# Kernel tuning notes

Measured on AMD Instinct MI355X. Metric: run time of the kernel, lower is better.

Reference implementation:

```python
import jax, jax.numpy as jnp
import numpy as np

B, C, P, N_PARTS, JOINTS_PER_PART = 2048, 256, 15, 5, 3
GROUPS = 4
EPS = 1e-5
MASK_VAL = 10000.0


def setup_inputs() -> dict:
    key = jax.random.key(0)
    k1, k2, k3 = jax.random.split(key, 3)
    g = (2 * C) // GROUPS  # 128
    return {
        "x": jax.random.normal(k1, (B, C, P, 1), jnp.float32),
        "conv_w": jax.random.normal(k2, (GROUPS, g, g), jnp.float32) * 0.05,
        "conv_b": jax.random.normal(k3, (2 * C,), jnp.float32) * 0.05,
        "bn_gamma": jnp.ones((2 * C,), jnp.float32),
        "bn_beta": jnp.zeros((2 * C,), jnp.float32),
    }


def reference(x, conv_w, conv_b, bn_gamma, bn_beta):
    Bb, Cc, Pp, _ = x.shape
    xs = x[..., 0]  # [B, C, P]

    # relative[b,c,i,k] = xs[b,c,k] - xs[b,c,i]; for a row i in part p the
    # reduction is max_k(relative - MASK_VAL * [k in part p]). Since the mask
    # only depends on the part of row i, precompute the per-part masked max of
    # xs over k and broadcast-subtract xs[i].
    part_id = jnp.arange(Pp) // JOINTS_PER_PART  # [P]
    Mg = jnp.where(part_id[None, :] == jnp.arange(N_PARTS)[:, None], -MASK_VAL, 0.0)  # [5, P]
    m = jnp.max(xs[:, :, None, :] + Mg[None, None, :, :], axis=-1)  # [B, C, 5]
    tmp = m[:, :, part_id] - xs  # [B, C, P]

    y = jnp.concatenate([xs, tmp], axis=1)  # [B, 2C, P]

    # grouped 1x1 conv (groups=4)
    g = (2 * Cc) // GROUPS
    y4 = y.reshape(Bb, GROUPS, g, Pp)
    z = jnp.einsum('bgip,goi->bgop', y4, conv_w).reshape(Bb, 2 * Cc, Pp)
    z = z + conv_b[None, :, None]

    # BatchNorm2d, training mode: biased batch stats over (B, spatial)
    mean = jnp.mean(z, axis=(0, 2))
    var = jnp.var(z, axis=(0, 2))
    zn = (z - mean[None, :, None]) * jax.lax.rsqrt(var + EPS)[None, :, None]
    out = jax.nn.relu(zn * bn_gamma[None, :, None] + bn_beta[None, :, None])
    return out[..., None]  # [B, 2C, P, 1]
```

## Files before the change

kernel.cpp:

```cpp
#include <hip/hip_runtime.h>
#include <hip/hip_bf16.h>
#include <cstdint>

#define EPS_ 1e-5f
#define NVALID_F 30720.0f

typedef __bf16 bf16x8 __attribute__((ext_vector_type(8)));
typedef float f32x16 __attribute__((ext_vector_type(16)));
typedef unsigned short u16x8 __attribute__((ext_vector_type(8)));
typedef float f32x4a4 __attribute__((ext_vector_type(4), aligned(4)));
typedef float f32x2a4 __attribute__((ext_vector_type(2), aligned(4)));

__device__ __forceinline__ unsigned short f2bf(float f) {
  unsigned u = __float_as_uint(f);
  u += 0x7FFFu + ((u >> 16) & 1u);
  return (unsigned short)(u >> 16);
}
__device__ __forceinline__ float bf2f(unsigned short h) {
  return __uint_as_float((unsigned)h << 16);
}

__global__ void k_wprep(const float* __restrict__ w, unsigned short* __restrict__ wf) {
  int q = blockIdx.x * 256 + threadIdx.x;
  int l = q & 63, ks = (q >> 6) & 7, mt = (q >> 9) & 3, g = q >> 11;
  int o = mt * 32 + (l & 31);
  int i = ks * 16 + (l >> 5) * 8;
  const float* src = w + ((size_t)(g * 128 + o) * 128 + i);
  u16x8 v;
#pragma unroll
  for (int j = 0; j < 8; ++j) v[j] = f2bf(src[j]);
  *(u16x8*)(wf + (size_t)q * 8) = v;
}

__device__ __forceinline__ void build_Y(const float* __restrict__ x, int b0, int t,
                                        unsigned short* __restrict__ Yt) {
#pragma unroll
  for (int bi = 0; bi < 2; ++bi) {
    const float* xb = x + (size_t)(b0 + bi) * 3840 + t * 15;
    f32x4a4 u0 = *(const f32x4a4*)(xb);
    f32x4a4 u1 = *(const f32x4a4*)(xb + 4);
    f32x4a4 u2 = *(const f32x4a4*)(xb + 8);
    f32x2a4 u3 = *(const f32x2a4*)(xb + 12);
    float u4 = xb[14];
    float v[15];
#pragma unroll
    for (int j = 0; j < 4; ++j) { v[j] = u0[j]; v[4 + j] = u1[j]; v[8 + j] = u2[j]; }
    v[12] = u3[0]; v[13] = u3[1]; v[14] = u4;
    float pm[5];
#pragma unroll
    for (int q = 0; q < 5; ++q) pm[q] = fmaxf(fmaxf(v[3 * q], v[3 * q + 1]), v[3 * q + 2]);
    float mq[5];
    mq[0] = fmaxf(fmaxf(pm[1], pm[2]), fmaxf(pm[3], pm[4]));
    mq[1] = fmaxf(fmaxf(pm[0], pm[2]), fmaxf(pm[3], pm[4]));
    mq[2] = fmaxf(fmaxf(pm[0], pm[1]), fmaxf(pm[3], pm[4]));
    mq[3] = fmaxf(fmaxf(pm[0], pm[1]), fmaxf(pm[2], pm[4]));
    mq[4] = fmaxf(fmaxf(pm[0], pm[1]), fmaxf(pm[2], pm[3]));
    const int c0 = bi * 16;
#pragma unroll
    for (int p = 0; p < 15; ++p) {
      Yt[(c0 + p) * 520 + t] = f2bf(v[p]);
      Yt[(c0 + p) * 520 + 256 + t] = f2bf(mq[p / 3] - v[p]);
    }
    Yt[(c0 + 15) * 520 + t] = 0;
    Yt[(c0 + 15) * 520 + 256 + t] = 0;
  }
}

__global__ __launch_bounds__(256, 3) void k_pass1(const float* __restrict__ x,
                                                  const unsigned short* __restrict__ wf,
                                                  float2* __restrict__ Part) {
  __shared__ unsigned short Yt[32 * 520];
  const int t = threadIdx.x;
  const int b0 = blockIdx.x * 2;
  build_Y(x, b0, t, Yt);
  __syncthreads();

  const int lane = t & 63, g = t >> 6;
  const int l31 = lane & 31, lh = lane >> 5;
  const bf16x8* Wfv = (const bf16x8*)wf;

  bf16x8 bfr[8];
  const unsigned short* yrow = &Yt[l31 * 520 + g * 128 + lh * 8];
#pragma unroll
  for (int ks = 0; ks < 8; ++ks)
    bfr[ks] = *(const bf16x8*)(yrow + ks * 16);

  bf16x8 wrA[8], wrB[8];
#pragma unroll
  for (int ks = 0; ks < 8; ++ks)
    wrA[ks] = Wfv[(size_t)((g * 4 + 0) * 8 + ks) * 64 + lane];

#define MT_STEP1(MT, CUR, NXT, PRE)                                             \
  do {                                                                          \
    if (PRE) {                                                                  \
      _Pragma("unroll") for (int ks = 0; ks < 8; ++ks)                          \
          NXT[ks] = Wfv[(size_t)((g * 4 + (MT) + 1) * 8 + ks) * 64 + lane];     \
    }                                                                           \
    f32x16 acc;                                                                 \
    _Pragma("unroll") for (int r = 0; r < 16; ++r) acc[r] = 0.f;                \
    _Pragma("unroll") for (int ks = 0; ks < 8; ++ks)                            \
        acc = __builtin_amdgcn_mfma_f32_32x32x16_bf16(bfr[ks], CUR[ks], acc, 0, 0, 0); \
    float s = 0.f, s2 = 0.f;                                                    \
    _Pragma("unroll") for (int r = 0; r < 16; ++r) {                            \
      float vv = acc[r]; s += vv; s2 = fmaf(vv, vv, s2);                        \
    }                                                                           \
    s += __shfl_xor(s, 32, 64);                                                 \
    s2 += __shfl_xor(s2, 32, 64);                                               \
    const int ch = g * 128 + (MT) * 32 + l31;                                   \
    if (lane < 32) Part[(size_t)blockIdx.x * 512 + ch] = make_float2(s, s2);    \
  } while (0)

  MT_STEP1(0, wrA, wrB, 1);
  MT_STEP1(1, wrB, wrA, 1);
  MT_STEP1(2, wrA, wrB, 1);
  MT_STEP1(3, wrB, wrA, 0);
#undef MT_STEP1
}

__global__ void k_stats(const float2* __restrict__ Part,
                        const float* __restrict__ gamma, const float* __restrict__ beta,
                        float2* __restrict__ AB) {
  const int ch = blockIdx.x, t = threadIdx.x;
  float s = 0.f, s2 = 0.f;
#pragma unroll
  for (int i = 0; i < 4; ++i) {
    float2 v = Part[(size_t)(t + 256 * i) * 512 + ch];
    s += v.x; s2 += v.y;
  }
#pragma unroll
  for (int m = 32; m >= 1; m >>= 1) { s += __shfl_xor(s, m, 64); s2 += __shfl_xor(s2, m, 64); }
  __shared__ float ls[4], ls2[4];
  if ((t & 63) == 0) { ls[t >> 6] = s; ls2[t >> 6] = s2; }
  __syncthreads();
  if (t == 0) {
    float S = ls[0] + ls[1] + ls[2] + ls[3];
    float S2 = ls2[0] + ls2[1] + ls2[2] + ls2[3];
    const float inv = 1.f / NVALID_F;
    float mean = S * inv;
    float var = fmaxf(S2 * inv - mean * mean, 0.f);
    float a = gamma[ch] * rsqrtf(var + EPS_);
    AB[ch] = make_float2(a, beta[ch] - mean * a);
  }
}

__global__ __launch_bounds__(256, 3) void k_pass2(const float* __restrict__ x,
                                                  const unsigned short* __restrict__ wf,
                                                  const float2* __restrict__ AB,
                                                  float* __restrict__ out) {
  __shared__ unsigned short Yt[32 * 520];
  __shared__ float aArr[512], bArr[512];
  const int t = threadIdx.x;
  const int b0 = blockIdx.x * 2;
  build_Y(x, b0, t, Yt);
  __syncthreads();

  {
    const int lane = t & 63, g = t >> 6;
    const int l31 = lane & 31, lh = lane >> 5;
    const bf16x8* Wfv = (const bf16x8*)wf;

    bf16x8 bfr[8];
    const unsigned short* yrow = &Yt[l31 * 520 + g * 128 + lh * 8];
#pragma unroll
    for (int ks = 0; ks < 8; ++ks)
      bfr[ks] = *(const bf16x8*)(yrow + ks * 16);
#pragma unroll
    for (int i = 0; i < 2; ++i) {
      int ch = i * 256 + t;
      float2 ab = AB[ch];
      aArr[ch] = ab.x; bArr[ch] = ab.y;
    }

    bf16x8 wrA[8], wrB[8];
#pragma unroll
    for (int ks = 0; ks < 8; ++ks)
      wrA[ks] = Wfv[(size_t)((g * 4 + 0) * 8 + ks) * 64 + lane];

#define MT_STEP2(MT, CUR, NXT, PRE)                                             \
  do {                                                                          \
    if (PRE) {                                                                  \
      _Pragma("unroll") for (int ks = 0; ks < 8; ++ks)                          \
          NXT[ks] = Wfv[(size_t)((g * 4 + (MT) + 1) * 8 + ks) * 64 + lane];     \
    }                                                                           \
    f32x16 acc;                                                                 \
    _Pragma("unroll") for (int r = 0; r < 16; ++r) acc[r] = 0.f;                \
    _Pragma("unroll") for (int ks = 0; ks < 8; ++ks)                            \
        acc = __builtin_amdgcn_mfma_f32_32x32x16_bf16(bfr[ks], CUR[ks], acc, 0, 0, 0); \
    const int ch = g * 128 + (MT) * 32 + l31;                                   \
    _Pragma("unroll") for (int r = 0; r < 16; ++r) {                            \
      int row = (r & 3) + 8 * (r >> 2) + 4 * lh;                                \
      Yt[row * 520 + ch] = f2bf(acc[r]);      \
    }                                                                           \
  } while (0)

    MT_STEP2(0, wrA, wrB, 1);
    MT_STEP2(1, wrB, wrA, 1);
    MT_STEP2(2, wrA, wrB, 1);
    MT_STEP2(3, wrB, wrA, 0);
#undef MT_STEP2
  }
  __syncthreads();

#pragma unroll
  for (int bi = 0; bi < 2; ++bi) {
    float2* slab = (float2*)(out + (size_t)(b0 + bi) * 7680);
#pragma unroll 5
    for (int k = 0; k < 15; ++k) {
      int e0 = k * 512 + 2 * t;
      int ch0 = e0 / 15, p0 = e0 - ch0 * 15;
      int e1 = e0 + 1;
      int ch1 = e1 / 15, p1 = e1 - ch1 * 15;
      float f0 = bf2f(Yt[(bi * 16 + p0) * 520 + ch0]);
      float f1 = bf2f(Yt[(bi * 16 + p1) * 520 + ch1]);
      slab[k * 256 + t] = make_float2(
          fmaxf(fmaf(f0, aArr[ch0], bArr[ch0]), 0.f),
          fmaxf(fmaf(f1, aArr[ch1], bArr[ch1]), 0.f));
    }
  }
}

extern "C" void kernel_launch(void* const* d_in, const int* in_sizes, int n_in,
                              void* d_out, int out_size, void* d_ws, size_t ws_size,
                              hipStream_t stream) {
  const float* x = (const float*)d_in[0];
  const float* cw = (const float*)d_in[1];
  const float* gamma = (const float*)d_in[3];
  const float* beta = (const float*)d_in[4];

  unsigned short* wf = (unsigned short*)d_ws;
  float2* Part = (float2*)(wf + 65536);
  float2* AB = Part + (size_t)1024 * 512;

  hipLaunchKernelGGL(k_wprep, dim3(32), dim3(256), 0, stream, cw, wf);
  hipLaunchKernelGGL(k_pass1, dim3(1024), dim3(256), 0, stream, x, wf, Part);
  hipLaunchKernelGGL(k_stats, dim3(512), dim3(256), 0, stream, Part, gamma, beta, AB);
  hipLaunchKernelGGL(k_pass2, dim3(1024), dim3(256), 0, stream, x, wf, AB, (float*)d_out);
}
```

Measured before the change: 48.54 us.

## Stage x through LDS with coalesced loads, drop weight double-buffering, batch stats channels

Input x for the two batch elements is copied into shared memory with coalesced 16-byte loads, then read back per thread, replacing per-thread strided global loads. The weight double-buffering macros become a simple loop over tiles, which lowers register pressure so launch bounds can go from 3 to 4 blocks per SM. k_stats now reduces 8 channels per block with coalesced reads over 64 blocks. The AB load in pass2 is moved before build. Costs are two extra barriers and weight-load latency that is no longer hidden by prefetch.

```diff
diff --git a/kernel.cpp b/kernel.cpp
--- a/kernel.cpp
+++ b/kernel.cpp
@@ -7,9 +7,8 @@
 
 typedef __bf16 bf16x8 __attribute__((ext_vector_type(8)));
 typedef float f32x16 __attribute__((ext_vector_type(16)));
+typedef float f32x4 __attribute__((ext_vector_type(4)));
 typedef unsigned short u16x8 __attribute__((ext_vector_type(8)));
-typedef float f32x4a4 __attribute__((ext_vector_type(4), aligned(4)));
-typedef float f32x2a4 __attribute__((ext_vector_type(2), aligned(4)));
 
 __device__ __forceinline__ unsigned short f2bf(float f) {
   unsigned u = __float_as_uint(f);
@@ -32,23 +31,27 @@
   *(u16x8*)(wf + (size_t)q * 8) = v;
 }
 
-__device__ __forceinline__ void build_Y(const float* __restrict__ x, int b0, int t,
-                                        unsigned short* __restrict__ Yt) {
+__device__ __forceinline__ void build_Y_union(const float* __restrict__ x, int b0, int t,
+                                              unsigned short* __restrict__ Yt) {
+  {
+    const f32x4* src = (const f32x4*)(x + (size_t)b0 * 3840);
+    f32x4* dst = (f32x4*)Yt;
+    for (int q = t; q < 1920; q += 256) dst[q] = src[q];
+  }
+  __syncthreads();
+  float v[2][15];
+  const float* xsf = (const float*)Yt;
+#pragma unroll
+  for (int bi = 0; bi < 2; ++bi)
+#pragma unroll
+    for (int p = 0; p < 15; ++p) v[bi][p] = xsf[bi * 3840 + t * 15 + p];
+  __syncthreads();
 #pragma unroll
   for (int bi = 0; bi < 2; ++bi) {
-    const float* xb = x + (size_t)(b0 + bi) * 3840 + t * 15;
-    f32x4a4 u0 = *(const f32x4a4*)(xb);
-    f32x4a4 u1 = *(const f32x4a4*)(xb + 4);
-    f32x4a4 u2 = *(const f32x4a4*)(xb + 8);
-    f32x2a4 u3 = *(const f32x2a4*)(xb + 12);
-    float u4 = xb[14];
-    float v[15];
-#pragma unroll
-    for (int j = 0; j < 4; ++j) { v[j] = u0[j]; v[4 + j] = u1[j]; v[8 + j] = u2[j]; }
-    v[12] = u3[0]; v[13] = u3[1]; v[14] = u4;
     float pm[5];
 #pragma unroll
-    for (int q = 0; q < 5; ++q) pm[q] = fmaxf(fmaxf(v[3 * q], v[3 * q + 1]), v[3 * q + 2]);
+    for (int q = 0; q < 5; ++q)
+      pm[q] = fmaxf(fmaxf(v[bi][3 * q], v[bi][3 * q + 1]), v[bi][3 * q + 2]);
     float mq[5];
     mq[0] = fmaxf(fmaxf(pm[1], pm[2]), fmaxf(pm[3], pm[4]));
     mq[1] = fmaxf(fmaxf(pm[0], pm[2]), fmaxf(pm[3], pm[4]));
@@ -58,21 +61,21 @@
     const int c0 = bi * 16;
 #pragma unroll
     for (int p = 0; p < 15; ++p) {
-      Yt[(c0 + p) * 520 + t] = f2bf(v[p]);
-      Yt[(c0 + p) * 520 + 256 + t] = f2bf(mq[p / 3] - v[p]);
+      Yt[(c0 + p) * 520 + t] = f2bf(v[bi][p]);
+      Yt[(c0 + p) * 520 + 256 + t] = f2bf(mq[p / 3] - v[bi][p]);
     }
     Yt[(c0 + 15) * 520 + t] = 0;
     Yt[(c0 + 15) * 520 + 256 + t] = 0;
   }
 }
 
-__global__ __launch_bounds__(256, 3) void k_pass1(const float* __restrict__ x,
+__global__ __launch_bounds__(256, 4) void k_pass1(const float* __restrict__ x,
                                                   const unsigned short* __restrict__ wf,
                                                   float2* __restrict__ Part) {
-  __shared__ unsigned short Yt[32 * 520];
+  __shared__ __align__(16) unsigned short Yt[32 * 520];
   const int t = threadIdx.x;
   const int b0 = blockIdx.x * 2;
-  build_Y(x, b0, t, Yt);
+  build_Y_union(x, b0, t, Yt);
   __syncthreads();
 
   const int lane = t & 63, g = t >> 6;
@@ -85,73 +88,72 @@
   for (int ks = 0; ks < 8; ++ks)
     bfr[ks] = *(const bf16x8*)(yrow + ks * 16);
 
-  bf16x8 wrA[8], wrB[8];
-#pragma unroll
-  for (int ks = 0; ks < 8; ++ks)
-    wrA[ks] = Wfv[(size_t)((g * 4 + 0) * 8 + ks) * 64 + lane];
-
-#define MT_STEP1(MT, CUR, NXT, PRE)                                             \
-  do {                                                                          \
-    if (PRE) {                                                                  \
-      _Pragma("unroll") for (int ks = 0; ks < 8; ++ks)                          \
-          NXT[ks] = Wfv[(size_t)((g * 4 + (MT) + 1) * 8 + ks) * 64 + lane];     \
-    }                                                                           \
-    f32x16 acc;                                                                 \
-    _Pragma("unroll") for (int r = 0; r < 16; ++r) acc[r] = 0.f;                \
-    _Pragma("unroll") for (int ks = 0; ks < 8; ++ks)                            \
-        acc = __builtin_amdgcn_mfma_f32_32x32x16_bf16(bfr[ks], CUR[ks], acc, 0, 0, 0); \
-    float s = 0.f, s2 = 0.f;                                                    \
-    _Pragma("unroll") for (int r = 0; r < 16; ++r) {                            \
-      float vv = acc[r]; s += vv; s2 = fmaf(vv, vv, s2);                        \
-    }                                                                           \
-    s += __shfl_xor(s, 32, 64);                                                 \
-    s2 += __shfl_xor(s2, 32, 64);                                               \
-    const int ch = g * 128 + (MT) * 32 + l31;                                   \
-    if (lane < 32) Part[(size_t)blockIdx.x * 512 + ch] = make_float2(s, s2);    \
-  } while (0)
-
-  MT_STEP1(0, wrA, wrB, 1);
-  MT_STEP1(1, wrB, wrA, 1);
-  MT_STEP1(2, wrA, wrB, 1);
-  MT_STEP1(3, wrB, wrA, 0);
-#undef MT_STEP1
+  for (int mt = 0; mt < 4; ++mt) {
+    bf16x8 wr[8];
+#pragma unroll
+    for (int ks = 0; ks < 8; ++ks)
+      wr[ks] = Wfv[(size_t)((g * 4 + mt) * 8 + ks) * 64 + lane];
+    f32x16 acc;
+#pragma unroll
+    for (int r = 0; r < 16; ++r) acc[r] = 0.f;
+#pragma unroll
+    for (int ks = 0; ks < 8; ++ks)
+      acc = __builtin_amdgcn_mfma_f32_32x32x16_bf16(bfr[ks], wr[ks], acc, 0, 0, 0);
+    float s = 0.f, s2 = 0.f;
+#pragma unroll
+    for (int r = 0; r < 16; ++r) { float vv = acc[r]; s += vv; s2 = fmaf(vv, vv, s2); }
+    s += __shfl_xor(s, 32, 64);
+    s2 += __shfl_xor(s2, 32, 64);
+    const int ch = g * 128 + mt * 32 + l31;
+    if (lane < 32) Part[(size_t)blockIdx.x * 512 + ch] = make_float2(s, s2);
+  }
 }
 
 __global__ void k_stats(const float2* __restrict__ Part,
                         const float* __restrict__ gamma, const float* __restrict__ beta,
                         float2* __restrict__ AB) {
-  const int ch = blockIdx.x, t = threadIdx.x;
+  const int t = threadIdx.x;
+  const int chb = blockIdx.x * 8;
+  const int c = t & 7, r0 = t >> 3;
   float s = 0.f, s2 = 0.f;
-#pragma unroll
-  for (int i = 0; i < 4; ++i) {
-    float2 v = Part[(size_t)(t + 256 * i) * 512 + ch];
-    s += v.x; s2 += v.y;
-  }
-#pragma unroll
-  for (int m = 32; m >= 1; m >>= 1) { s += __shfl_xor(s, m, 64); s2 += __shfl_xor(s2, m, 64); }
-  __shared__ float ls[4], ls2[4];
-  if ((t & 63) == 0) { ls[t >> 6] = s; ls2[t >> 6] = s2; }
-  __syncthreads();
-  if (t == 0) {
-    float S = ls[0] + ls[1] + ls[2] + ls[3];
-    float S2 = ls2[0] + ls2[1] + ls2[2] + ls2[3];
+  for (int k = 0; k < 32; ++k) {
+    float2 vv = Part[(size_t)(r0 + 32 * k) * 512 + chb + c];
+    s += vv.x; s2 += vv.y;
+  }
+  s += __shfl_xor(s, 8, 64);  s2 += __shfl_xor(s2, 8, 64);
+  s += __shfl_xor(s, 16, 64); s2 += __shfl_xor(s2, 16, 64);
+  s += __shfl_xor(s, 32, 64); s2 += __shfl_xor(s2, 32, 64);
+  __shared__ float2 red[4][8];
+  if ((t & 63) < 8) red[t >> 6][c] = make_float2(s, s2);
+  __syncthreads();
+  if (t < 8) {
+    float S = 0.f, S2 = 0.f;
+#pragma unroll
+    for (int w = 0; w < 4; ++w) { S += red[w][t].x; S2 += red[w][t].y; }
     const float inv = 1.f / NVALID_F;
     float mean = S * inv;
     float var = fmaxf(S2 * inv - mean * mean, 0.f);
-    float a = gamma[ch] * rsqrtf(var + EPS_);
-    AB[ch] = make_float2(a, beta[ch] - mean * a);
-  }
-}
-
-__global__ __launch_bounds__(256, 3) void k_pass2(const float* __restrict__ x,
+    float a = gamma[chb + t] * rsqrtf(var + EPS_);
+    AB[chb + t] = make_float2(a, beta[chb + t] - mean * a);
+  }
+}
+
+__global__ __launch_bounds__(256, 4) void k_pass2(const float* __restrict__ x,
                                                   const unsigned short* __restrict__ wf,
                                                   const float2* __restrict__ AB,
                                                   float* __restrict__ out) {
-  __shared__ unsigned short Yt[32 * 520];
+  __shared__ __align__(16) unsigned short Yt[32 * 520];
   __shared__ float aArr[512], bArr[512];
   const int t = threadIdx.x;
   const int b0 = blockIdx.x * 2;
-  build_Y(x, b0, t, Yt);
+
+#pragma unroll
+  for (int i = 0; i < 2; ++i) {
+    int ch = i * 256 + t;
+    float2 ab = AB[ch];
+    aArr[ch] = ab.x; bArr[ch] = ab.y;
+  }
+  build_Y_union(x, b0, t, Yt);
   __syncthreads();
 
   {
@@ -164,40 +166,25 @@
 #pragma unroll
     for (int ks = 0; ks < 8; ++ks)
       bfr[ks] = *(const bf16x8*)(yrow + ks * 16);
-#pragma unroll
-    for (int i = 0; i < 2; ++i) {
-      int ch = i * 256 + t;
-      float2 ab = AB[ch];
-      aArr[ch] = ab.x; bArr[ch] = ab.y;
+
+    for (int mt = 0; mt < 4; ++mt) {
+      bf16x8 wr[8];
+#pragma unroll
+      for (int ks = 0; ks < 8; ++ks)
+        wr[ks] = Wfv[(size_t)((g * 4 + mt) * 8 + ks) * 64 + lane];
+      f32x16 acc;
+#pragma unroll
+      for (int r = 0; r < 16; ++r) acc[r] = 0.f;
+#pragma unroll
+      for (int ks = 0; ks < 8; ++ks)
+        acc = __builtin_amdgcn_mfma_f32_32x32x16_bf16(bfr[ks], wr[ks], acc, 0, 0, 0);
+      const int ch = g * 128 + mt * 32 + l31;
+#pragma unroll
+      for (int r = 0; r < 16; ++r) {
+        int row = (r & 3) + 8 * (r >> 2) + 4 * lh;
+        Yt[row * 520 + ch] = f2bf(acc[r]);
+      }
     }
-
-    bf16x8 wrA[8], wrB[8];
-#pragma unroll
-    for (int ks = 0; ks < 8; ++ks)
-      wrA[ks] = Wfv[(size_t)((g * 4 + 0) * 8 + ks) * 64 + lane];
-
-#define MT_STEP2(MT, CUR, NXT, PRE)                                             \
-  do {                                                                          \
-    if (PRE) {                                                                  \
-      _Pragma("unroll") for (int ks = 0; ks < 8; ++ks)                          \
-          NXT[ks] = Wfv[(size_t)((g * 4 + (MT) + 1) * 8 + ks) * 64 + lane];     \
-    }                                                                           \
-    f32x16 acc;                                                                 \
-    _Pragma("unroll") for (int r = 0; r < 16; ++r) acc[r] = 0.f;                \
-    _Pragma("unroll") for (int ks = 0; ks < 8; ++ks)                            \
-        acc = __builtin_amdgcn_mfma_f32_32x32x16_bf16(bfr[ks], CUR[ks], acc, 0, 0, 0); \
-    const int ch = g * 128 + (MT) * 32 + l31;                                   \
-    _Pragma("unroll") for (int r = 0; r < 16; ++r) {                            \
-      int row = (r & 3) + 8 * (r >> 2) + 4 * lh;                                \
-      Yt[row * 520 + ch] = f2bf(acc[r]);      \
-    }                                                                           \
-  } while (0)
-
-    MT_STEP2(0, wrA, wrB, 1);
-    MT_STEP2(1, wrB, wrA, 1);
-    MT_STEP2(2, wrA, wrB, 1);
-    MT_STEP2(3, wrB, wrA, 0);
-#undef MT_STEP2
   }
   __syncthreads();
 
@@ -233,6 +220,6 @@
 
   hipLaunchKernelGGL(k_wprep, dim3(32), dim3(256), 0, stream, cw, wf);
   hipLaunchKernelGGL(k_pass1, dim3(1024), dim3(256), 0, stream, x, wf, Part);
-  hipLaunchKernelGGL(k_stats, dim3(512), dim3(256), 0, stream, Part, gamma, beta, AB);
+  hipLaunchKernelGGL(k_stats, dim3(64), dim3(256), 0, stream, Part, gamma, beta, AB);
   hipLaunchKernelGGL(k_pass2, dim3(1024), dim3(256), 0, stream, x, wf, AB, (float*)d_out);
 }
```

After: 48.27 us. About the same (-0.6%).
